# Optimization experiments

Hardware: AMD Instinct MI355X
Metric: run time of the kernel (lower is better)

## Reference

```python
import jax, jax.numpy as jnp
import numpy as np

HEADS = 16
DIM_HEAD = 64
QUERY_DIM = 1024
INNER_DIM = HEADS * DIM_HEAD  # 1024
SCALE = DIM_HEAD ** (-0.5)


def setup_inputs() -> dict:
    key = jax.random.key(0)
    ks = jax.random.split(key, 6)
    B, S = 4, 2048
    hidden_states = jax.random.normal(ks[0], (B, S, QUERY_DIM), dtype=jnp.float32)
    # Linear weights stored as [in, out] for x @ W convention
    init = 1.0 / np.sqrt(QUERY_DIM)
    Wq = jax.random.uniform(ks[1], (QUERY_DIM, INNER_DIM), jnp.float32, -init, init)
    Wk = jax.random.uniform(ks[2], (QUERY_DIM, INNER_DIM), jnp.float32, -init, init)
    Wv = jax.random.uniform(ks[3], (QUERY_DIM, INNER_DIM), jnp.float32, -init, init)
    Wo = jax.random.uniform(ks[4], (INNER_DIM, QUERY_DIM), jnp.float32, -init, init)
    bo = jax.random.uniform(ks[5], (QUERY_DIM,), jnp.float32, -init, init)
    return {"hidden_states": hidden_states, "Wq": Wq, "Wk": Wk, "Wv": Wv, "Wo": Wo, "bo": bo}


def reference(hidden_states, Wq, Wk, Wv, Wo, bo):
    B, S, _ = hidden_states.shape
    # Projections
    q = hidden_states @ Wq  # [B,S,inner]
    k = hidden_states @ Wk
    v = hidden_states @ Wv
    # [B, H, S, D]
    q = q.reshape(B, S, HEADS, DIM_HEAD).transpose(0, 2, 1, 3)
    k = k.reshape(B, S, HEADS, DIM_HEAD).transpose(0, 2, 1, 3)
    v = v.reshape(B, S, HEADS, DIM_HEAD).transpose(0, 2, 1, 3)
    # Attention scores and softmax (scale after matmul, as in source)
    scores = jnp.einsum('bhqd,bhkd->bhqk', q, k) * SCALE
    attn = jax.nn.softmax(scores, axis=-1)
    out = jnp.einsum('bhqk,bhkd->bhqd', attn, v)  # [B,H,S,D]
    out = out.transpose(0, 2, 1, 3).reshape(B, S, INNER_DIM)
    return out @ Wo + bo
```

## Files before the change

### kernel.cpp

```cpp
#include <hip/hip_runtime.h>
#include <stdint.h>

typedef short v8s __attribute__((ext_vector_type(8)));
typedef float v4f __attribute__((ext_vector_type(4)));
typedef unsigned int u32;
typedef unsigned short us;

#define LOG2E 1.44269504088896340736f

__device__ __forceinline__ u32 f2u(float x) {
  union { float f; u32 u; } t; t.f = x; return t.u;
}

__device__ __forceinline__ unsigned short bfr(float x) {
  u32 u = f2u(x);
  u32 r = u + 0x7FFFu + ((u >> 16) & 1u);
  return (unsigned short)(r >> 16);
}

__device__ __forceinline__ u32 pk2(float a, float b) {
  return __builtin_amdgcn_perm(f2u(b) + 0x8000u, f2u(a) + 0x8000u, 0x07060302u);
}

__device__ __forceinline__ void async16(const void* g, void* l) {
  __builtin_amdgcn_global_load_lds(
      (const __attribute__((address_space(1))) u32*)g,
      (__attribute__((address_space(3))) u32*)l, 16, 0, 0);
}

#define MFMA_K32(A, B, C) __builtin_amdgcn_mfma_f32_16x16x32_bf16((A), (B), (C), 0, 0, 0)

__global__ void cast_h_kernel(const float4* __restrict__ in, ushort4* __restrict__ out, int n4) {
  int i = blockIdx.x * blockDim.x + threadIdx.x;
  if (i < n4) {
    float4 v = in[i];
    ushort4 o;
    o.x = bfr(v.x); o.y = bfr(v.y); o.z = bfr(v.z); o.w = bfr(v.w);
    out[i] = o;
  }
}

__global__ void transpose_cast4_kernel(const float* __restrict__ W0, const float* __restrict__ W1,
                                       const float* __restrict__ W2, const float* __restrict__ W3,
                                       us* __restrict__ O0, us* __restrict__ O1,
                                       us* __restrict__ O2, us* __restrict__ O3) {
  __shared__ float tile[32][33];
  const int z = blockIdx.z;
  const float* in = (z == 0) ? W0 : (z == 1) ? W1 : (z == 2) ? W2 : W3;
  us* out = (z == 0) ? O0 : (z == 1) ? O1 : (z == 2) ? O2 : O3;
  const float scale = (z == 0) ? 0.125f * LOG2E : 1.0f;
  const int N = 1024;
  int n0 = blockIdx.x * 32, k0 = blockIdx.y * 32;
  int tx = threadIdx.x, ty = threadIdx.y;
#pragma unroll
  for (int j = 0; j < 32; j += 8)
    tile[ty + j][tx] = in[(size_t)(k0 + ty + j) * N + n0 + tx];
  __syncthreads();
#pragma unroll
  for (int j = 0; j < 32; j += 8)
    out[(size_t)(n0 + ty + j) * 1024 + k0 + tx] = bfr(tile[tx][ty + j] * scale);
}

template <int MODE>
__global__ __launch_bounds__(256)
void gemm_bt_kernel(const us* __restrict__ A, const us* __restrict__ Bt,
                    us* __restrict__ dQ, us* __restrict__ dK, us* __restrict__ dV,
                    float* __restrict__ outF, const float* __restrict__ bias) {
  __shared__ __align__(16) us sm[MODE == 3 ? 16896 : 16384];
  us* As = sm;
  us* Bs = sm + 8192;
  const int tid = threadIdx.x;
  const int wid = tid >> 6;
  const int lane = tid & 63;
  const int quad = lane >> 4;
  const int l16 = lane & 15;
  const int tile_m = blockIdx.y * 128;
  const int tile_n = blockIdx.x * 128;
  const bool vpath = (MODE == 3) && (tile_n >= 2048);

  const int srow = wid * 32 + (lane >> 3);
  const int sc = lane & 7;

  v4f zero = {0.f, 0.f, 0.f, 0.f};
  v4f acc[4][4];
#pragma unroll
  for (int i = 0; i < 4; ++i)
#pragma unroll
    for (int j = 0; j < 4; ++j) acc[i][j] = zero;

  const int wm = (wid >> 1) * 64;
  const int wn = (wid & 1) * 64;

  for (int k0 = 0; k0 < 1024; k0 += 64) {
#pragma unroll
    for (int it = 0; it < 4; ++it) {
      int rr = srow + it * 8;
      int cg = sc ^ (rr & 7);
      async16(A + (size_t)(tile_m + rr) * 1024 + k0 + cg * 8, &As[rr * 64 + sc * 8]);
      async16(Bt + (size_t)(tile_n + rr) * 1024 + k0 + cg * 8, &Bs[rr * 64 + sc * 8]);
    }
    __syncthreads();
#pragma unroll
    for (int ks = 0; ks < 2; ++ks) {
      v8s a[4], b[4];
#pragma unroll
      for (int i = 0; i < 4; ++i) {
        int row = wm + i * 16 + l16;
        a[i] = *(const v8s*)&As[row * 64 + (((ks * 4 + quad) ^ (row & 7)) * 8)];
      }
#pragma unroll
      for (int j = 0; j < 4; ++j) {
        int row = wn + j * 16 + l16;
        b[j] = *(const v8s*)&Bs[row * 64 + (((ks * 4 + quad) ^ (row & 7)) * 8)];
      }
      if (vpath) {
#pragma unroll
        for (int i = 0; i < 4; ++i)
#pragma unroll
          for (int j = 0; j < 4; ++j)
            acc[i][j] = MFMA_K32(a[i], b[j], acc[i][j]);
      } else {
#pragma unroll
        for (int i = 0; i < 4; ++i)
#pragma unroll
          for (int j = 0; j < 4; ++j)
            acc[i][j] = MFMA_K32(b[j], a[i], acc[i][j]);
      }
    }
    __syncthreads();
  }

  if (MODE == 2) {
#pragma unroll
    for (int i = 0; i < 4; ++i) {
      int row = tile_m + wm + i * 16 + l16;
#pragma unroll
      for (int j = 0; j < 4; ++j) {
        int col = tile_n + wn + j * 16 + quad * 4;
        float4 bv = *(const float4*)&bias[col];
        float4 o;
        o.x = acc[i][j][0] + bv.x; o.y = acc[i][j][1] + bv.y;
        o.z = acc[i][j][2] + bv.z; o.w = acc[i][j][3] + bv.w;
        *(float4*)&outF[(size_t)row * 1024 + col] = o;
      }
    }
  } else if (!vpath) {
    us* base = (tile_n < 1024) ? dQ : dK;
    const int coln = tile_n & 1023;
#pragma unroll
    for (int i = 0; i < 4; ++i) {
      int row = tile_m + wm + i * 16 + l16;
      int b_ = row >> 11, s_ = row & 2047;
#pragma unroll
      for (int j = 0; j < 4; ++j) {
        int col = coln + wn + j * 16 + quad * 4;
        int h = (col >> 6) & 15, d = col & 63;
        uint2 pk = make_uint2(pk2(acc[i][j][0], acc[i][j][1]), pk2(acc[i][j][2], acc[i][j][3]));
        *(uint2*)&base[((size_t)(b_ * 16 + h) * 2048 + s_) * 64 + d] = pk;
      }
    }
  } else {
    const int vn = tile_n - 2048;
#pragma unroll
    for (int i = 0; i < 4; ++i) {
      int sp = wm + (i >> 1) * 32 + quad * 8 + (i & 1) * 4;
#pragma unroll
      for (int j = 0; j < 4; ++j) {
        int col = wn + j * 16 + l16;
        uint2 pk = make_uint2(pk2(acc[i][j][0], acc[i][j][1]), pk2(acc[i][j][2], acc[i][j][3]));
        *(uint2*)&sm[col * 132 + sp] = pk;
      }
    }
    __syncthreads();
    const int b_ = tile_m >> 11;
    const int sbase = tile_m & 2047;
#pragma unroll
    for (int it = 0; it < 8; ++it) {
      int u = it * 256 + tid;
      int col = u >> 4, sp = (u & 15) * 8;
      v8s val = *(const v8s*)&sm[col * 132 + sp];
      int colg = vn + col;
      int h = (colg >> 6) & 15, d = colg & 63;
      *(v8s*)&dV[((size_t)(b_ * 16 + h) * 64 + d) * 2048 + sbase + sp] = val;
    }
  }
}

__global__ __launch_bounds__(256, 2)
void flash_kernel(const us* __restrict__ Q, const us* __restrict__ K,
                  const us* __restrict__ Vt, us* __restrict__ O) {
  __shared__ __align__(16) us sm[16384];
  us* Ks = sm;
  us* Vts = sm + 8192;

  const int tid = threadIdx.x;
  const int wid = tid >> 6;
  const int lane = tid & 63;
  const int quad = lane >> 4;
  const int l16 = lane & 15;
  const int id = blockIdx.x;
  const int bh = id & 63;
  const int q0 = (id >> 6) * 256;
  const int wq = wid * 64;
  const us* Qp = Q + (size_t)bh * (2048 * 64);
  const us* Kp = K + (size_t)bh * (2048 * 64);
  const us* Vp = Vt + (size_t)bh * (64 * 2048);

  v8s qB[4][2];
#pragma unroll
  for (int mi = 0; mi < 4; ++mi)
#pragma unroll
    for (int ks = 0; ks < 2; ++ks)
      qB[mi][ks] = *(const v8s*)&Qp[(size_t)(q0 + wq + mi * 16 + l16) * 64 + ks * 32 + quad * 8];

  v4f zero = {0.f, 0.f, 0.f, 0.f};
  v4f o[4][4];
#pragma unroll
  for (int i = 0; i < 4; ++i)
#pragma unroll
    for (int mi = 0; mi < 4; ++mi) o[i][mi] = zero;
  v4f l_acc[4] = {zero, zero, zero, zero};
  const us one_bf = 0x3F80;
  const v8s ones = {(short)one_bf, (short)one_bf, (short)one_bf, (short)one_bf,
                    (short)one_bf, (short)one_bf, (short)one_bf, (short)one_bf};

  for (int kv0 = 0; kv0 < 2048; kv0 += 128) {
    __syncthreads();
    {
      int r0 = wid * 32 + (lane >> 3);
      int c = lane & 7;
#pragma unroll
      for (int it = 0; it < 4; ++it) {
        int rr = r0 + it * 8;
        int cg = c ^ (rr & 7);
        async16(Kp + (size_t)(kv0 + rr) * 64 + cg * 8, &Ks[rr * 64 + c * 8]);
      }
    }
    {
      int d0 = wid * 16 + (lane >> 4);
      int c = lane & 15;
#pragma unroll
      for (int it = 0; it < 4; ++it) {
        int dd = d0 + it * 4;
        int cg = c ^ (dd & 15);
        async16(Vp + (size_t)dd * 2048 + kv0 + cg * 8, &Vts[dd * 128 + c * 8]);
      }
    }
    __syncthreads();

#pragma unroll
    for (int hf = 0; hf < 2; ++hf) {
      v4f sT[4][4];
#pragma unroll
      for (int m = 0; m < 4; ++m)
#pragma unroll
        for (int mi = 0; mi < 4; ++mi) sT[m][mi] = zero;
#pragma unroll
      for (int ks = 0; ks < 2; ++ks) {
        v8s kA[4];
#pragma unroll
        for (int m = 0; m < 4; ++m) {
          int kvr = hf * 64 + m * 16 + l16;
          int cc = (ks * 4 + quad) ^ (l16 & 7);
          kA[m] = *(const v8s*)&Ks[kvr * 64 + cc * 8];
        }
#pragma unroll
        for (int m = 0; m < 4; ++m)
#pragma unroll
          for (int mi = 0; mi < 4; ++mi)
            sT[m][mi] = MFMA_K32(kA[m], qB[mi][ks], sT[m][mi]);
      }

#pragma unroll
      for (int cp = 0; cp < 2; ++cp) {
        v8s bp[4];
#pragma unroll
        for (int mi = 0; mi < 4; ++mi) {
          union { u32 w[4]; v8s s; } u;
#pragma unroll
          for (int dm = 0; dm < 2; ++dm) {
            int m = cp * 2 + dm;
            float p0 = __builtin_amdgcn_exp2f(sT[m][mi][0]);
            float p1 = __builtin_amdgcn_exp2f(sT[m][mi][1]);
            float p2 = __builtin_amdgcn_exp2f(sT[m][mi][2]);
            float p3 = __builtin_amdgcn_exp2f(sT[m][mi][3]);
            u.w[dm * 2] = pk2(p0, p1);
            u.w[dm * 2 + 1] = pk2(p2, p3);
          }
          bp[mi] = u.s;
          l_acc[mi] = MFMA_K32(ones, bp[mi], l_acc[mi]);
        }
#pragma unroll
        for (int i = 0; i < 4; ++i) {
          int d = i * 16 + l16;
          int cc = (hf * 8 + cp * 4 + quad) ^ (d & 15);
          v8s vt = *(const v8s*)&Vts[d * 128 + cc * 8];
#pragma unroll
          for (int mi = 0; mi < 4; ++mi)
            o[i][mi] = MFMA_K32(vt, bp[mi], o[i][mi]);
        }
      }
    }
  }

  float invl[4];
#pragma unroll
  for (int mi = 0; mi < 4; ++mi) invl[mi] = 1.0f / l_acc[mi][0];

  __syncthreads();
#pragma unroll
  for (int mi = 0; mi < 4; ++mi) {
    int q = wq + mi * 16 + l16;
#pragma unroll
    for (int i = 0; i < 4; ++i)
#pragma unroll
      for (int rp = 0; rp < 4; rp += 2) {
        int d = i * 16 + quad * 4 + rp;
        u32 pk = pk2(o[i][mi][rp] * invl[mi], o[i][mi][rp + 1] * invl[mi]);
        *(u32*)&sm[q * 64 + ((d >> 3) ^ (q & 7)) * 8 + (d & 7)] = pk;
      }
  }
  __syncthreads();
  const int b_ = bh >> 4, h_ = bh & 15;
#pragma unroll
  for (int it = 0; it < 8; ++it) {
    int u = it * 256 + tid;
    int row = u >> 3, ch = u & 7;
    v8s val = *(const v8s*)&sm[row * 64 + (ch ^ (row & 7)) * 8];
    *(v8s*)&O[((size_t)(b_ * 2048 + q0 + row)) * 1024 + h_ * 64 + ch * 8] = val;
  }
}

extern "C" void kernel_launch(void* const* d_in, const int* in_sizes, int n_in,
                              void* d_out, int out_size, void* d_ws, size_t ws_size,
                              hipStream_t stream) {
  const float* Hs = (const float*)d_in[0];
  const float* Wq = (const float*)d_in[1];
  const float* Wk = (const float*)d_in[2];
  const float* Wv = (const float*)d_in[3];
  const float* Wo = (const float*)d_in[4];
  const float* bo = (const float*)d_in[5];
  float* out = (float*)d_out;
  char* ws = (char*)d_ws;
  const size_t MiB = 1ull << 20;
  us* Hb  = (us*)(ws);
  us* Wqt = (us*)(ws + 16 * MiB);
  us* Wkt = (us*)(ws + 18 * MiB);
  us* Wvt = (us*)(ws + 20 * MiB);
  us* Wot = (us*)(ws + 22 * MiB);
  us* Qb  = (us*)(ws + 24 * MiB);
  us* Kb  = (us*)(ws + 40 * MiB);
  us* Vtb = (us*)(ws + 56 * MiB);
  us* Ob  = Hb;
  (void)Wkt; (void)Wvt;

  cast_h_kernel<<<8192, 256, 0, stream>>>((const float4*)Hs, (ushort4*)Hb, 2097152);
  transpose_cast4_kernel<<<dim3(32, 32, 4), dim3(32, 8), 0, stream>>>(Wq, Wk, Wv, Wo,
                                                                      Wqt, Wkt, Wvt, Wot);
  gemm_bt_kernel<3><<<dim3(24, 64), 256, 0, stream>>>(Hb, Wqt, Qb, Kb, Vtb, nullptr, nullptr);
  flash_kernel<<<512, 256, 0, stream>>>(Qb, Kb, Vtb, Ob);
  gemm_bt_kernel<2><<<dim3(8, 64), 256, 0, stream>>>(Ob, Wot, nullptr, nullptr, nullptr, out, bo);
}
```

Baseline: 257.9 us.

## Load K/V fragments directly from global in flash kernel; fuse prep kernels

The flash attention kernel no longer stages K and V^T tiles in shared memory with async copies and barriers. Each wave now loads its MFMA operand fragments straight from global memory. The separate input cast and weight transpose kernels are merged into one launch, cutting launch overhead. The trade-off is that the four waves of a block each fetch the same K/V data, which relies on cache hits and exposes global load latency.

```diff
diff --git a/kernel.cpp b/kernel.cpp
--- a/kernel.cpp
+++ b/kernel.cpp
@@ -30,31 +30,31 @@
 
 #define MFMA_K32(A, B, C) __builtin_amdgcn_mfma_f32_16x16x32_bf16((A), (B), (C), 0, 0, 0)
 
-__global__ void cast_h_kernel(const float4* __restrict__ in, ushort4* __restrict__ out, int n4) {
-  int i = blockIdx.x * blockDim.x + threadIdx.x;
-  if (i < n4) {
-    float4 v = in[i];
+__global__ void prep_kernel(const float4* __restrict__ Hs4, ushort4* __restrict__ Hb4,
+                            const float* __restrict__ W0, const float* __restrict__ W1,
+                            const float* __restrict__ W2, const float* __restrict__ W3,
+                            us* __restrict__ O0, us* __restrict__ O1,
+                            us* __restrict__ O2, us* __restrict__ O3) {
+  __shared__ float tile[32][33];
+  const int blk = blockIdx.x;
+  if (blk < 8192) {
+    int i = blk * 256 + threadIdx.x;
+    float4 v = Hs4[i];
     ushort4 o;
     o.x = bfr(v.x); o.y = bfr(v.y); o.z = bfr(v.z); o.w = bfr(v.w);
-    out[i] = o;
-  }
-}
-
-__global__ void transpose_cast4_kernel(const float* __restrict__ W0, const float* __restrict__ W1,
-                                       const float* __restrict__ W2, const float* __restrict__ W3,
-                                       us* __restrict__ O0, us* __restrict__ O1,
-                                       us* __restrict__ O2, us* __restrict__ O3) {
-  __shared__ float tile[32][33];
-  const int z = blockIdx.z;
+    Hb4[i] = o;
+    return;
+  }
+  const int zb = blk - 8192;
+  const int z = zb >> 10;
   const float* in = (z == 0) ? W0 : (z == 1) ? W1 : (z == 2) ? W2 : W3;
   us* out = (z == 0) ? O0 : (z == 1) ? O1 : (z == 2) ? O2 : O3;
   const float scale = (z == 0) ? 0.125f * LOG2E : 1.0f;
-  const int N = 1024;
-  int n0 = blockIdx.x * 32, k0 = blockIdx.y * 32;
-  int tx = threadIdx.x, ty = threadIdx.y;
+  const int n0 = ((zb >> 5) & 31) * 32, k0 = (zb & 31) * 32;
+  const int tx = threadIdx.x & 31, ty = threadIdx.x >> 5;
 #pragma unroll
   for (int j = 0; j < 32; j += 8)
-    tile[ty + j][tx] = in[(size_t)(k0 + ty + j) * N + n0 + tx];
+    tile[ty + j][tx] = in[(size_t)(k0 + ty + j) * 1024 + n0 + tx];
   __syncthreads();
 #pragma unroll
   for (int j = 0; j < 32; j += 8)
@@ -190,8 +190,6 @@
 void flash_kernel(const us* __restrict__ Q, const us* __restrict__ K,
                   const us* __restrict__ Vt, us* __restrict__ O) {
   __shared__ __align__(16) us sm[16384];
-  us* Ks = sm;
-  us* Vts = sm + 8192;
 
   const int tid = threadIdx.x;
   const int wid = tid >> 6;
@@ -224,30 +222,12 @@
   const v8s ones = {(short)one_bf, (short)one_bf, (short)one_bf, (short)one_bf,
                     (short)one_bf, (short)one_bf, (short)one_bf, (short)one_bf};
 
+  const us* kb = Kp + (size_t)l16 * 64 + quad * 8;
+  const us* vb = Vp + (size_t)l16 * 2048 + quad * 8;
+
   for (int kv0 = 0; kv0 < 2048; kv0 += 128) {
-    __syncthreads();
-    {
-      int r0 = wid * 32 + (lane >> 3);
-      int c = lane & 7;
-#pragma unroll
-      for (int it = 0; it < 4; ++it) {
-        int rr = r0 + it * 8;
-        int cg = c ^ (rr & 7);
-        async16(Kp + (size_t)(kv0 + rr) * 64 + cg * 8, &Ks[rr * 64 + c * 8]);
-      }
-    }
-    {
-      int d0 = wid * 16 + (lane >> 4);
-      int c = lane & 15;
-#pragma unroll
-      for (int it = 0; it < 4; ++it) {
-        int dd = d0 + it * 4;
-        int cg = c ^ (dd & 15);
-        async16(Vp + (size_t)dd * 2048 + kv0 + cg * 8, &Vts[dd * 128 + c * 8]);
-      }
-    }
-    __syncthreads();
-
+    const us* kt = kb + (size_t)kv0 * 64;
+    const us* vt0 = vb + kv0;
 #pragma unroll
     for (int hf = 0; hf < 2; ++hf) {
       v4f sT[4][4];
@@ -259,11 +239,8 @@
       for (int ks = 0; ks < 2; ++ks) {
         v8s kA[4];
 #pragma unroll
-        for (int m = 0; m < 4; ++m) {
-          int kvr = hf * 64 + m * 16 + l16;
-          int cc = (ks * 4 + quad) ^ (l16 & 7);
-          kA[m] = *(const v8s*)&Ks[kvr * 64 + cc * 8];
-        }
+        for (int m = 0; m < 4; ++m)
+          kA[m] = *(const v8s*)&kt[hf * 4096 + m * 1024 + ks * 32];
 #pragma unroll
         for (int m = 0; m < 4; ++m)
 #pragma unroll
@@ -273,6 +250,10 @@
 
 #pragma unroll
       for (int cp = 0; cp < 2; ++cp) {
+        v8s vv[4];
+#pragma unroll
+        for (int i = 0; i < 4; ++i)
+          vv[i] = *(const v8s*)&vt0[i * 32768 + hf * 64 + cp * 32];
         v8s bp[4];
 #pragma unroll
         for (int mi = 0; mi < 4; ++mi) {
@@ -291,14 +272,10 @@
           l_acc[mi] = MFMA_K32(ones, bp[mi], l_acc[mi]);
         }
 #pragma unroll
-        for (int i = 0; i < 4; ++i) {
-          int d = i * 16 + l16;
-          int cc = (hf * 8 + cp * 4 + quad) ^ (d & 15);
-          v8s vt = *(const v8s*)&Vts[d * 128 + cc * 8];
+        for (int i = 0; i < 4; ++i)
 #pragma unroll
           for (int mi = 0; mi < 4; ++mi)
-            o[i][mi] = MFMA_K32(vt, bp[mi], o[i][mi]);
-        }
+            o[i][mi] = MFMA_K32(vv[i], bp[mi], o[i][mi]);
       }
     }
   }
@@ -307,7 +284,6 @@
 #pragma unroll
   for (int mi = 0; mi < 4; ++mi) invl[mi] = 1.0f / l_acc[mi][0];
 
-  __syncthreads();
 #pragma unroll
   for (int mi = 0; mi < 4; ++mi) {
     int q = wq + mi * 16 + l16;
@@ -354,9 +330,8 @@
   us* Ob  = Hb;
   (void)Wkt; (void)Wvt;
 
-  cast_h_kernel<<<8192, 256, 0, stream>>>((const float4*)Hs, (ushort4*)Hb, 2097152);
-  transpose_cast4_kernel<<<dim3(32, 32, 4), dim3(32, 8), 0, stream>>>(Wq, Wk, Wv, Wo,
-                                                                      Wqt, Wkt, Wvt, Wot);
+  prep_kernel<<<12288, 256, 0, stream>>>((const float4*)Hs, (ushort4*)Hb,
+                                         Wq, Wk, Wv, Wo, Wqt, Wkt, Wvt, Wot);
   gemm_bt_kernel<3><<<dim3(24, 64), 256, 0, stream>>>(Hb, Wqt, Qb, Kb, Vtb, nullptr, nullptr);
   flash_kernel<<<512, 256, 0, stream>>>(Qb, Kb, Vtb, Ob);
   gemm_bt_kernel<2><<<dim3(8, 64), 256, 0, stream>>>(Ob, Wot, nullptr, nullptr, nullptr, out, bo);
```

After: 304.7 us. +18.2%, slower.
